# Kernel tuning notes

Hardware: AMD Instinct MI355X
Metric: run time of the kernel (lower is better)

## Reference

```python
import jax, jax.numpy as jnp
import numpy as np

TAU = 0.95
MARGIN = 1.0
NUM_NEG = 1

B, S = 4096, 4096
N_RERANK = 8192


def setup_inputs() -> dict:
    key = jax.random.key(0)
    k1, k2, k3 = jax.random.split(key, 3)
    rerank_y = jax.random.normal(k1, (N_RERANK, 1), dtype=jnp.float32)
    # probabilities in (0,1]; keep away from 0 since the loss takes log
    cut_y = jax.random.uniform(k2, (B, S, 1), dtype=jnp.float32, minval=1e-4, maxval=1.0)
    rerank_label = jnp.ones((B, 1), dtype=jnp.float32)  # unused (overwritten by ones in source)
    cut_label = jax.random.randint(k3, (B, S), 0, 2, dtype=jnp.int32)
    return {"rerank_y": rerank_y, "cut_y": cut_y, "rerank_label": rerank_label, "cut_label": cut_label}


def _f1_weights(cut_label):
    # Vectorized Metric_for_Loss.f1(labels[i], j): F1 at cut depth j+1.
    lab = cut_label.astype(jnp.float32)                      # [B,S]
    cum = jnp.cumsum(lab, axis=1)                            # relevant docs within top j+1
    k = jnp.arange(1, lab.shape[1] + 1, dtype=jnp.float32)   # cut depth
    total = jnp.sum(lab, axis=1, keepdims=True)              # total relevant per list
    prec = cum / k
    rec = jnp.where(total > 0, cum / jnp.maximum(total, 1.0), 0.0)
    den = prec + rec
    return jnp.where(den > 0, 2.0 * prec * rec / den, 0.0)   # [B,S]


def _attncut_loss(cut_y, cut_label):
    out2d = jnp.squeeze(cut_y, axis=2)                       # [B,S]
    r = _f1_weights(cut_label)
    # Faithful to source: q = exp(r/tau) is summed into norm_factor, then q := 1/norm_factor
    norm = jnp.sum(jnp.exp(r / TAU), axis=1, keepdims=True)  # [B,1]
    q = 1.0 / norm
    loss_mat = jnp.log(out2d) * q
    return -jnp.sum(loss_mat) / out2d.shape[0]


def _rerank_loss(rerank_y):
    y_pos = rerank_y[:: NUM_NEG + 1, :]                      # [B,1]
    y_neg = rerank_y[1 :: NUM_NEG + 1, :]                    # [B,1] (num_neg=1 -> cat of one)
    y_neg = jnp.mean(y_neg, axis=-1, keepdims=True)
    # margin_ranking_loss with y=1, reduction='mean'
    return jnp.mean(jnp.maximum(0.0, -(y_pos - y_neg) + MARGIN))


def reference(rerank_y, cut_y, rerank_label, cut_label):
    return _attncut_loss(cut_y, cut_label) + _rerank_loss(rerank_y)
```

## Files before the change

### kernel.cpp

```cpp
#include <hip/hip_runtime.h>

#define NROWS 4096
#define NCOLS 4096
#define TAU 0.95f
#define MARGIN 1.0f

__global__ __launch_bounds__(256) void fused_kernel(
    const float* __restrict__ cut_y, const int* __restrict__ cut_label,
    float* __restrict__ norm_out, float* __restrict__ logsum_out) {
  const int t = threadIdx.x;
  const int lane = t & 63;
  const int wid = t >> 6;
  __shared__ float red[4];
  __shared__ int wsum[4];

  if (blockIdx.x < NROWS) {
    const int row = blockIdx.x;
    const float4* Yp = (const float4*)(cut_y + (size_t)row * NCOLS);
    const float4 a0 = Yp[t];
    const float4 a1 = Yp[t + 256];
    const float4 a2 = Yp[t + 512];
    const float4 a3 = Yp[t + 768];
    float s = __logf(a0.x) + __logf(a0.y) + __logf(a0.z) + __logf(a0.w) +
              __logf(a1.x) + __logf(a1.y) + __logf(a1.z) + __logf(a1.w) +
              __logf(a2.x) + __logf(a2.y) + __logf(a2.z) + __logf(a2.w) +
              __logf(a3.x) + __logf(a3.y) + __logf(a3.z) + __logf(a3.w);
#pragma unroll
    for (int off = 32; off > 0; off >>= 1) s += __shfl_down(s, off, 64);
    if (lane == 0) red[wid] = s;
    __syncthreads();
    if (t == 0) logsum_out[row] = (red[0] + red[1]) + (red[2] + red[3]);
  } else {
    const int row = blockIdx.x - NROWS;
    const int4* Lp = (const int4*)(cut_label + (size_t)row * NCOLS) + t * 4;
    const int4 L0 = Lp[0], L1 = Lp[1], L2 = Lp[2], L3 = Lp[3];

    const int lsum = L0.x + L0.y + L0.z + L0.w + L1.x + L1.y + L1.z + L1.w +
                     L2.x + L2.y + L2.z + L2.w + L3.x + L3.y + L3.z + L3.w;

    int x = lsum;
#pragma unroll
    for (int off = 1; off < 64; off <<= 1) {
      int v = __shfl_up(x, off, 64);
      if (lane >= off) x += v;
    }
    if (lane == 63) wsum[wid] = x;
    __syncthreads();
    int prev = 0;
#pragma unroll
    for (int w = 0; w < 4; ++w)
      if (w < wid) prev += wsum[w];
    const int Ttot = wsum[0] + wsum[1] + wsum[2] + wsum[3];
    int c = prev + x - lsum;

    const float Tf = (float)Ttot;
    const float kbase = (float)(t * 16);
    float norm_acc = 0.f;

#define STEP(LAB, J)                                                     \
  {                                                                      \
    c += (LAB);                                                          \
    float r = __fdividef(2.0f * (float)c, kbase + (float)((J) + 1) + Tf);\
    r = (c > 0) ? r : 0.0f;                                              \
    norm_acc += __expf(r * (1.0f / TAU));                                \
  }
    STEP(L0.x, 0)  STEP(L0.y, 1)  STEP(L0.z, 2)  STEP(L0.w, 3)
    STEP(L1.x, 4)  STEP(L1.y, 5)  STEP(L1.z, 6)  STEP(L1.w, 7)
    STEP(L2.x, 8)  STEP(L2.y, 9)  STEP(L2.z, 10) STEP(L2.w, 11)
    STEP(L3.x, 12) STEP(L3.y, 13) STEP(L3.z, 14) STEP(L3.w, 15)
#undef STEP

#pragma unroll
    for (int off = 32; off > 0; off >>= 1)
      norm_acc += __shfl_down(norm_acc, off, 64);
    if (lane == 0) red[wid] = norm_acc;
    __syncthreads();
    if (t == 0) norm_out[row] = (red[0] + red[1]) + (red[2] + red[3]);
  }
}

__global__ __launch_bounds__(256) void finish_kernel(
    const float* __restrict__ norms, const float* __restrict__ logsums,
    const float* __restrict__ rerank_y, float* __restrict__ out) {
  const int t = threadIdx.x;
  const int lane = t & 63, wid = t >> 6;

  float acc = 0.f;
  const float4* n4 = (const float4*)norms;
  const float4* l4 = (const float4*)logsums;
#pragma unroll
  for (int i = 0; i < 4; ++i) {
    const float4 n = n4[t + 256 * i];
    const float4 l = l4[t + 256 * i];
    acc += __fdividef(l.x, n.x) + __fdividef(l.y, n.y) +
           __fdividef(l.z, n.z) + __fdividef(l.w, n.w);
  }
  acc *= -(1.0f / (float)NROWS);

  float racc = 0.f;
  const float4* y4 = (const float4*)rerank_y;
#pragma unroll
  for (int i = 0; i < 8; ++i) {
    const float4 v = y4[t + 256 * i];
    racc += fmaxf(0.f, MARGIN - (v.x - v.y));
    racc += fmaxf(0.f, MARGIN - (v.z - v.w));
  }
  acc += racc * (1.0f / 4096.0f);

#pragma unroll
  for (int off = 32; off > 0; off >>= 1) acc += __shfl_down(acc, off, 64);
  __shared__ float ws[4];
  if (lane == 0) ws[wid] = acc;
  __syncthreads();
  if (t == 0) out[0] = (ws[0] + ws[1]) + (ws[2] + ws[3]);
}

extern "C" void kernel_launch(void* const* d_in, const int* in_sizes, int n_in,
                              void* d_out, int out_size, void* d_ws, size_t ws_size,
                              hipStream_t stream) {
  const float* rerank_y = (const float*)d_in[0];
  const float* cut_y = (const float*)d_in[1];
  const int* cut_label = (const int*)d_in[3];
  float* out = (float*)d_out;
  float* norms = (float*)d_ws;
  float* logsums = (float*)d_ws + NROWS;

  fused_kernel<<<2 * NROWS, 256, 0, stream>>>(cut_y, cut_label, norms, logsums);
  finish_kernel<<<1, 256, 0, stream>>>(norms, logsums, rerank_y, out);
}
```

Baseline: 154.9 us.

## Assign one wavefront per row and pack labels into bitmasks

Each wavefront now handles a whole row instead of each block handling one, so the block-level shared-memory reductions and __syncthreads disappear and the grid shrinks fourfold. Labels are packed into 64-bit masks per lane, and the scan uses popcount plus a wave-only prefix. Log and exp are rewritten in base-2 form with constants folded in. Each lane now does 64 serial exp/divide steps, which lengthens the per-lane dependent chain, and the per-lane loads are strided differently for labels, which may affect coalescing.

```diff
diff --git a/kernel.cpp b/kernel.cpp
--- a/kernel.cpp
+++ b/kernel.cpp
@@ -4,78 +4,88 @@
 #define NCOLS 4096
 #define TAU 0.95f
 #define MARGIN 1.0f
+#define LN2F 0.6931471805599453f
 
 __global__ __launch_bounds__(256) void fused_kernel(
     const float* __restrict__ cut_y, const int* __restrict__ cut_label,
     float* __restrict__ norm_out, float* __restrict__ logsum_out) {
-  const int t = threadIdx.x;
-  const int lane = t & 63;
-  const int wid = t >> 6;
-  __shared__ float red[4];
-  __shared__ int wsum[4];
+  const int wid = threadIdx.x >> 6;
+  const int lane = threadIdx.x & 63;
+  const int row = (blockIdx.x >> 1) * 4 + wid;
 
-  if (blockIdx.x < NROWS) {
-    const int row = blockIdx.x;
+  if ((blockIdx.x & 1) == 0) {
     const float4* Yp = (const float4*)(cut_y + (size_t)row * NCOLS);
-    const float4 a0 = Yp[t];
-    const float4 a1 = Yp[t + 256];
-    const float4 a2 = Yp[t + 512];
-    const float4 a3 = Yp[t + 768];
-    float s = __logf(a0.x) + __logf(a0.y) + __logf(a0.z) + __logf(a0.w) +
-              __logf(a1.x) + __logf(a1.y) + __logf(a1.z) + __logf(a1.w) +
-              __logf(a2.x) + __logf(a2.y) + __logf(a2.z) + __logf(a2.w) +
-              __logf(a3.x) + __logf(a3.y) + __logf(a3.z) + __logf(a3.w);
+    float s0 = 0.f, s1 = 0.f, s2 = 0.f, s3 = 0.f;
+#define LOG4(V) (__log2f((V).x) + __log2f((V).y) + __log2f((V).z) + __log2f((V).w))
+#pragma unroll
+    for (int i = 0; i < 4; ++i) {
+      const float4 a = Yp[lane + 64 * (4 * i + 0)];
+      const float4 b = Yp[lane + 64 * (4 * i + 1)];
+      const float4 c = Yp[lane + 64 * (4 * i + 2)];
+      const float4 d = Yp[lane + 64 * (4 * i + 3)];
+      s0 += LOG4(a);
+      s1 += LOG4(b);
+      s2 += LOG4(c);
+      s3 += LOG4(d);
+    }
+#undef LOG4
+    float s = (s0 + s1) + (s2 + s3);
 #pragma unroll
     for (int off = 32; off > 0; off >>= 1) s += __shfl_down(s, off, 64);
-    if (lane == 0) red[wid] = s;
-    __syncthreads();
-    if (t == 0) logsum_out[row] = (red[0] + red[1]) + (red[2] + red[3]);
+    if (lane == 0) logsum_out[row] = s * LN2F;
   } else {
-    const int row = blockIdx.x - NROWS;
-    const int4* Lp = (const int4*)(cut_label + (size_t)row * NCOLS) + t * 4;
-    const int4 L0 = Lp[0], L1 = Lp[1], L2 = Lp[2], L3 = Lp[3];
+    const int4* Lp = (const int4*)(cut_label + (size_t)row * NCOLS) + lane * 16;
+    unsigned mlo = 0u, mhi = 0u;
+#pragma unroll
+    for (int i = 0; i < 4; ++i) {
+      const int4 a = Lp[4 * i + 0];
+      const int4 b = Lp[4 * i + 1];
+      const int4 c = Lp[4 * i + 2];
+      const int4 d = Lp[4 * i + 3];
+      const unsigned na = (unsigned)a.x | ((unsigned)a.y << 1) |
+                          ((unsigned)a.z << 2) | ((unsigned)a.w << 3);
+      const unsigned nb = (unsigned)b.x | ((unsigned)b.y << 1) |
+                          ((unsigned)b.z << 2) | ((unsigned)b.w << 3);
+      const unsigned nc = (unsigned)c.x | ((unsigned)c.y << 1) |
+                          ((unsigned)c.z << 2) | ((unsigned)c.w << 3);
+      const unsigned nd = (unsigned)d.x | ((unsigned)d.y << 1) |
+                          ((unsigned)d.z << 2) | ((unsigned)d.w << 3);
+      const unsigned group = na | (nb << 4) | (nc << 8) | (nd << 12);
+      if (i < 2)
+        mlo |= group << (16 * i);
+      else
+        mhi |= group << (16 * (i - 2));
+    }
+    const int cnt = __popc(mlo) + __popc(mhi);
 
-    const int lsum = L0.x + L0.y + L0.z + L0.w + L1.x + L1.y + L1.z + L1.w +
-                     L2.x + L2.y + L2.z + L2.w + L3.x + L3.y + L3.z + L3.w;
-
-    int x = lsum;
+    int x = cnt;
 #pragma unroll
     for (int off = 1; off < 64; off <<= 1) {
-      int v = __shfl_up(x, off, 64);
+      const int v = __shfl_up(x, off, 64);
       if (lane >= off) x += v;
     }
-    if (lane == 63) wsum[wid] = x;
-    __syncthreads();
-    int prev = 0;
-#pragma unroll
-    for (int w = 0; w < 4; ++w)
-      if (w < wid) prev += wsum[w];
-    const int Ttot = wsum[0] + wsum[1] + wsum[2] + wsum[3];
-    int c = prev + x - lsum;
+    const int Ttot = __shfl(x, 63, 64);
+    int c = x - cnt;
 
     const float Tf = (float)Ttot;
-    const float kbase = (float)(t * 16);
-    float norm_acc = 0.f;
-
-#define STEP(LAB, J)                                                     \
-  {                                                                      \
-    c += (LAB);                                                          \
-    float r = __fdividef(2.0f * (float)c, kbase + (float)((J) + 1) + Tf);\
-    r = (c > 0) ? r : 0.0f;                                              \
-    norm_acc += __expf(r * (1.0f / TAU));                                \
-  }
-    STEP(L0.x, 0)  STEP(L0.y, 1)  STEP(L0.z, 2)  STEP(L0.w, 3)
-    STEP(L1.x, 4)  STEP(L1.y, 5)  STEP(L1.z, 6)  STEP(L1.w, 7)
-    STEP(L2.x, 8)  STEP(L2.y, 9)  STEP(L2.z, 10) STEP(L2.w, 11)
-    STEP(L3.x, 12) STEP(L3.y, 13) STEP(L3.z, 14) STEP(L3.w, 15)
-#undef STEP
-
+    const float C2 = 2.0f / (TAU * LN2F);
+    const float kb = (float)(lane * 64 + 1) + Tf;
+    float acc0 = 0.f, acc1 = 0.f;
 #pragma unroll
-    for (int off = 32; off > 0; off >>= 1)
-      norm_acc += __shfl_down(norm_acc, off, 64);
-    if (lane == 0) red[wid] = norm_acc;
-    __syncthreads();
-    if (t == 0) norm_out[row] = (red[0] + red[1]) + (red[2] + red[3]);
+    for (int j = 0; j < 64; ++j) {
+      const unsigned w = (j < 32) ? mlo : mhi;
+      c += (int)((w >> (j & 31)) & 1u);
+      const float term =
+          __builtin_amdgcn_exp2f(__fdividef((float)c * C2, kb + (float)j));
+      if (j & 1)
+        acc1 += term;
+      else
+        acc0 += term;
+    }
+    float norm = acc0 + acc1;
+#pragma unroll
+    for (int off = 32; off > 0; off >>= 1) norm += __shfl_down(norm, off, 64);
+    if (lane == 0) norm_out[row] = norm;
   }
 }
 
@@ -125,6 +135,7 @@
   float* norms = (float*)d_ws;
   float* logsums = (float*)d_ws + NROWS;
 
-  fused_kernel<<<2 * NROWS, 256, 0, stream>>>(cut_y, cut_label, norms, logsums);
+  fused_kernel<<<2 * (NROWS / 4), 256, 0, stream>>>(cut_y, cut_label, norms,
+                                                    logsums);
   finish_kernel<<<1, 256, 0, stream>>>(norms, logsums, rerank_y, out);
 }
```

Result: slower. 163.2 us (+5.4%).
